# Optimization experiments

Hardware: AMD Instinct MI355X
Metric: run time of the kernel (lower is better)

The kernel has to match this reference:

```python
import jax, jax.numpy as jnp
import numpy as np

B, S = 8, 2048

def setup_inputs() -> dict:
    key = jax.random.key(0)
    ks = iter(jax.random.split(key, 64))
    def lin(din, dout):
        w = jax.random.normal(next(ks), (din, dout), jnp.float32) / np.float32(np.sqrt(din))
        b = jax.random.normal(next(ks), (dout,), jnp.float32) * 0.01
        return w, b
    inp = {}
    inp['x'] = jax.random.normal(next(ks), (B, S, 256), jnp.float32)
    def blk(tag, d, ff):
        for name, (din, dout) in [('q',(d,d)),('k',(d,d)),('v',(d,d)),('o',(d,d)),('ff1',(d,ff)),('ff2',(ff,d))]:
            w, b = lin(din, dout)
            inp[f'{name}_w{tag}'] = w; inp[f'{name}_b{tag}'] = b
        inp[f'ln1_g{tag}'] = jnp.ones((d,), jnp.float32); inp[f'ln1_b{tag}'] = jnp.zeros((d,), jnp.float32)
        inp[f'ln2_g{tag}'] = jnp.ones((d,), jnp.float32); inp[f'ln2_b{tag}'] = jnp.zeros((d,), jnp.float32)
    blk(1, 256, 1024)
    blk(2, 128, 512)
    for nm, (din, dout) in [('dr1',(256,128)),('dr2',(128,64)),('dr3',(64,32)),('dr4',(32,14))]:
        w, b = lin(din, dout)
        inp[f'{nm}_w'] = w; inp[f'{nm}_b'] = b
    return inp

def _ln(x, g, b, eps=1e-5):
    m = x.mean(-1, keepdims=True)
    v = ((x - m) ** 2).mean(-1, keepdims=True)
    return (x - m) / jnp.sqrt(v + eps) * g + b

def _mha(x, wq, bq, wk, bk, wv, bv, wo, bo, h):
    Bx, Sx, D = x.shape
    hd = D // h
    q = (x @ wq + bq).reshape(Bx, Sx, h, hd).transpose(0, 2, 1, 3)
    k = (x @ wk + bk).reshape(Bx, Sx, h, hd).transpose(0, 2, 1, 3)
    v = (x @ wv + bv).reshape(Bx, Sx, h, hd).transpose(0, 2, 1, 3)
    scores = jnp.einsum('bhqd,bhkd->bhqk', q, k) / jnp.sqrt(jnp.float32(hd))  # [B,h,S,S]
    p = jax.nn.softmax(scores, axis=-1)
    o = jnp.einsum('bhqk,bhkd->bqhd', p, v).reshape(Bx, Sx, D)
    return o @ wo + bo

def _encoder(x, p, h):
    a = _mha(x, p['qw'], p['qb'], p['kw'], p['kb'], p['vw'], p['vb'], p['ow'], p['ob'], h)
    x = _ln(a + x, p['g1'], p['b1'])
    f = jax.nn.relu(x @ p['fw1'] + p['fb1']) @ p['fw2'] + p['fb2']
    return _ln(f + x, p['g2'], p['b2'])

def _pe(s, d):
    pos = jnp.arange(s, dtype=jnp.float32)[:, None]
    dep = jnp.arange(d, dtype=jnp.float32)[None, :]
    ang = pos / jnp.power(jnp.float32(10000.0), dep / d)
    even = (jnp.arange(d)[None, :] % 2) == 0
    return jnp.where(even, jnp.sin(ang), jnp.cos(ang))

def _forward(x,
             q_w1, q_b1, k_w1, k_b1, v_w1, v_b1, o_w1, o_b1,
             ff1_w1, ff1_b1, ff2_w1, ff2_b1, ln1_g1, ln1_b1, ln2_g1, ln2_b1,
             dr1_w, dr1_b,
             q_w2, q_b2, k_w2, k_b2, v_w2, v_b2, o_w2, o_b2,
             ff1_w2, ff1_b2, ff2_w2, ff2_b2, ln1_g2, ln1_b2, ln2_g2, ln2_b2,
             dr2_w, dr2_b, dr3_w, dr3_b, dr4_w, dr4_b):
    h = x + _pe(x.shape[1], x.shape[2])
    p1 = dict(qw=q_w1, qb=q_b1, kw=k_w1, kb=k_b1, vw=v_w1, vb=v_b1, ow=o_w1, ob=o_b1,
              fw1=ff1_w1, fb1=ff1_b1, fw2=ff2_w1, fb2=ff2_b1, g1=ln1_g1, b1=ln1_b1, g2=ln2_g1, b2=ln2_b1)
    h = _encoder(h, p1, 8)
    h = h @ dr1_w + dr1_b
    p2 = dict(qw=q_w2, qb=q_b2, kw=k_w2, kb=k_b2, vw=v_w2, vb=v_b2, ow=o_w2, ob=o_b2,
              fw1=ff1_w2, fb1=ff1_b2, fw2=ff2_w2, fb2=ff2_b2, g1=ln1_g2, b1=ln1_b2, g2=ln2_g2, b2=ln2_b2)
    h = _encoder(h, p2, 8)
    h = h @ dr2_w + dr2_b
    h = jnp.max(h, axis=1)  # AdaptiveMaxPool1d(1) over the sequence dim -> [B, 64]
    h = h @ dr3_w + dr3_b
    return h @ dr4_w + dr4_b  # [B, 14]

def reference(x,
              q_w1, q_b1, k_w1, k_b1, v_w1, v_b1, o_w1, o_b1,
              ff1_w1, ff1_b1, ff2_w1, ff2_b1, ln1_g1, ln1_b1, ln2_g1, ln2_b1,
              dr1_w, dr1_b,
              q_w2, q_b2, k_w2, k_b2, v_w2, v_b2, o_w2, o_b2,
              ff1_w2, ff1_b2, ff2_w2, ff2_b2, ln1_g2, ln1_b2, ln2_g2, ln2_b2,
              dr2_w, dr2_b, dr3_w, dr3_b, dr4_w, dr4_b):
    return _forward(x,
                    q_w1, q_b1, k_w1, k_b1, v_w1, v_b1, o_w1, o_b1,
                    ff1_w1, ff1_b1, ff2_w1, ff2_b1, ln1_g1, ln1_b1, ln2_g1, ln2_b1,
                    dr1_w, dr1_b,
                    q_w2, q_b2, k_w2, k_b2, v_w2, v_b2, o_w2, o_b2,
                    ff1_w2, ff1_b2, ff2_w2, ff2_b2, ln1_g2, ln1_b2, ln2_g2, ln2_b2,
                    dr2_w, dr2_b, dr3_w, dr3_b, dr4_w, dr4_b)
```

## Files before the change

kernel.cpp:

```cpp
#include <hip/hip_runtime.h>
#include <hip/hip_bf16.h>
#include <math.h>

#define SEQ  2048
#define BATCH 8
#define NTOK (SEQ*BATCH)

typedef __attribute__((ext_vector_type(8))) short short8v;
typedef __attribute__((ext_vector_type(4))) float f32x4;
typedef unsigned short u16;

__device__ __forceinline__ u16 f2bf(float f) {
    __hip_bfloat16 h = __float2bfloat16(f);
    return *reinterpret_cast<u16*>(&h);
}

struct WDescs {
    const float* src[13];
    int K[13];
    int N[13];
    long dst[13];
    float scale[13];
    int tstart[14];
};

__global__ __launch_bounds__(256) void convert_w_kernel(WDescs d, u16* __restrict__ WA) {
    __shared__ float tile[64][65];
    int blk = blockIdx.x;
    int di = 0;
    while (di < 12 && blk >= d.tstart[di + 1]) ++di;
    int t  = blk - d.tstart[di];
    int K  = d.K[di], N = d.N[di];
    int tn = N >> 6;
    int k0 = (t / tn) << 6, n0 = (t % tn) << 6;
    const float* src = d.src[di];
    float sc = d.scale[di];
    int tid = threadIdx.x;
    #pragma unroll
    for (int i = 0; i < 16; ++i) {
        int id = i * 256 + tid;
        int kk = id >> 6, nn = id & 63;
        tile[kk][nn] = src[(size_t)(k0 + kk) * N + n0 + nn];
    }
    __syncthreads();
    u16* dst = WA + d.dst[di];
    #pragma unroll
    for (int i = 0; i < 16; ++i) {
        int id = i * 256 + tid;
        int nn = id >> 6, kk = id & 63;
        dst[(size_t)(n0 + nn) * K + k0 + kk] = f2bf(tile[kk][nn] * sc);
    }
}

__global__ __launch_bounds__(256) void convert_bias_kernel(
    const float* qb1, const float* kb1, const float* vb1,
    const float* qb2, const float* kb2, const float* vb2,
    float* __restrict__ BA, float qs1, float qs2)
{
    int t = blockIdx.x * 256 + threadIdx.x;
    if      (t < 256)  BA[t] = qb1[t] * qs1;
    else if (t < 512)  BA[t] = kb1[t - 256];
    else if (t < 768)  BA[t] = vb1[t - 512];
    else if (t < 896)  BA[t] = qb2[t - 768] * qs2;
    else if (t < 1024) BA[t] = kb2[t - 896];
    else if (t < 1152) BA[t] = vb2[t - 1024];
}

__global__ __launch_bounds__(256) void add_pe_kernel(const float* __restrict__ x,
                                                     float* __restrict__ h,
                                                     u16* __restrict__ hb) {
    int idx = blockIdx.x * 256 + threadIdx.x;
    int s = idx >> 8;
    int d = idx & 255;
    float p   = powf(10000.0f, (float)d * (1.0f / 256.0f));
    float ang = (float)s / p;
    float pe  = (d & 1) ? cosf(ang) : sinf(ang);
    #pragma unroll
    for (int b = 0; b < BATCH; ++b) {
        size_t g = ((size_t)(b * SEQ + s) << 8) + d;
        float v = x[g] + pe;
        h[g]  = v;
        hb[g] = f2bf(v);
    }
}

template<int RELU, int WF32, int WBF16>
__global__ __launch_bounds__(256) void gemm_bf16_kernel(
    const u16* __restrict__ A, const u16* __restrict__ Bt,
    const float* __restrict__ bias, float* __restrict__ Cf,
    u16* __restrict__ Cb, int N, int K)
{
    __shared__ u16 As[2][128 * 64];
    __shared__ u16 Bs[2][128 * 64];
    const int tid  = threadIdx.x;
    const int lane = tid & 63;
    const int c    = lane & 15, g = lane >> 4;
    const int w    = tid >> 6;
    const int wr   = w >> 1, wc = w & 1;
    const size_t bm = (size_t)blockIdx.y * 128;
    const size_t bn = (size_t)blockIdx.x * 128;

    f32x4 acc[4][4];
    #pragma unroll
    for (int i = 0; i < 4; ++i)
        #pragma unroll
        for (int j = 0; j < 4; ++j) acc[i][j] = (f32x4){0.f, 0.f, 0.f, 0.f};

    auto stage = [&](int buf, int t) {
        #pragma unroll
        for (int j = 0; j < 4; ++j) {
            int cid = j * 256 + tid;
            int row = cid >> 3, blk = cid & 7;
            int lofs = row * 64 + ((blk ^ (row & 7)) * 8);
            short8v av = *(const short8v*)&A[(bm + row) * K + t * 64 + blk * 8];
            *(short8v*)&As[buf][lofs] = av;
            short8v bv = *(const short8v*)&Bt[(bn + row) * K + t * 64 + blk * 8];
            *(short8v*)&Bs[buf][lofs] = bv;
        }
    };

    const int nt = K >> 6;
    stage(0, 0);
    __syncthreads();
    for (int t = 0; t < nt; ++t) {
        if (t + 1 < nt) stage((t + 1) & 1, t + 1);
        const int bfi = t & 1;
        #pragma unroll
        for (int ks2 = 0; ks2 < 2; ++ks2) {
            short8v af[4], bfr[4];
            #pragma unroll
            for (int am = 0; am < 4; ++am) {
                int r = wr * 64 + am * 16 + c;
                af[am] = *(const short8v*)&As[bfi][r * 64 + (((ks2 * 4 + g) ^ (r & 7)) * 8)];
            }
            #pragma unroll
            for (int bn_ = 0; bn_ < 4; ++bn_) {
                int r = wc * 64 + bn_ * 16 + c;
                bfr[bn_] = *(const short8v*)&Bs[bfi][r * 64 + (((ks2 * 4 + g) ^ (r & 7)) * 8)];
            }
            #pragma unroll
            for (int am = 0; am < 4; ++am)
                #pragma unroll
                for (int bn_ = 0; bn_ < 4; ++bn_)
                    acc[am][bn_] = __builtin_amdgcn_mfma_f32_16x16x32_bf16(
                                       af[am], bfr[bn_], acc[am][bn_], 0, 0, 0);
        }
        __syncthreads();
    }

    float bv[4];
    #pragma unroll
    for (int bn_ = 0; bn_ < 4; ++bn_) bv[bn_] = bias[bn + wc * 64 + bn_ * 16 + c];
    #pragma unroll
    for (int am = 0; am < 4; ++am) {
        #pragma unroll
        for (int bn_ = 0; bn_ < 4; ++bn_) {
            #pragma unroll
            for (int i = 0; i < 4; ++i) {
                size_t row = bm + wr * 64 + am * 16 + 4 * g + i;
                size_t col = bn + wc * 64 + bn_ * 16 + c;
                float v = acc[am][bn_][i] + bv[bn_];
                if (RELU) v = fmaxf(v, 0.f);
                if (WF32)  Cf[row * N + col] = v;
                if (WBF16) Cb[row * N + col] = f2bf(v);
            }
        }
    }
}

template<int RELU>
__global__ __launch_bounds__(256) void gemm_bias_kernel(
    const float* __restrict__ A, const float* __restrict__ W,
    const float* __restrict__ bias, float* __restrict__ C,
    int M, int N, int K)
{
    __shared__ float As[16][72];
    __shared__ float Bs[16][72];
    const int bm  = blockIdx.y * 64;
    const int bn  = blockIdx.x * 64;
    const int tid = threadIdx.x;
    const int tx  = tid & 15, ty = tid >> 4;

    float acc[4][4] = {{0.f}};

    for (int k0 = 0; k0 < K; k0 += 16) {
        #pragma unroll
        for (int i = 0; i < 4; ++i) {
            int f = tid + 256 * i;
            int row = f >> 4, kk = f & 15;
            As[kk][row] = A[(size_t)(bm + row) * K + k0 + kk];
        }
        #pragma unroll
        for (int i = 0; i < 4; ++i) {
            int f = tid + 256 * i;
            int kk = f >> 6, n = f & 63;
            Bs[kk][n] = W[(size_t)(k0 + kk) * N + bn + n];
        }
        __syncthreads();
        #pragma unroll
        for (int kk = 0; kk < 16; ++kk) {
            float4 a4 = *(const float4*)&As[kk][ty * 4];
            float4 b4 = *(const float4*)&Bs[kk][tx * 4];
            float av[4] = {a4.x, a4.y, a4.z, a4.w};
            float bw[4] = {b4.x, b4.y, b4.z, b4.w};
            #pragma unroll
            for (int i = 0; i < 4; ++i)
                #pragma unroll
                for (int j = 0; j < 4; ++j)
                    acc[i][j] = fmaf(av[i], bw[j], acc[i][j]);
        }
        __syncthreads();
    }

    float4 b4 = *(const float4*)&bias[bn + tx * 4];
    float bw[4] = {b4.x, b4.y, b4.z, b4.w};
    #pragma unroll
    for (int i = 0; i < 4; ++i) {
        int row = bm + ty * 4 + i;
        float4 o;
        float v0 = acc[i][0] + bw[0];
        float v1 = acc[i][1] + bw[1];
        float v2 = acc[i][2] + bw[2];
        float v3 = acc[i][3] + bw[3];
        if (RELU) {
            v0 = fmaxf(v0, 0.f); v1 = fmaxf(v1, 0.f);
            v2 = fmaxf(v2, 0.f); v3 = fmaxf(v3, 0.f);
        }
        o.x = v0; o.y = v1; o.z = v2; o.w = v3;
        *(float4*)&C[(size_t)row * N + bn + tx * 4] = o;
    }
}

template<int D, int WBF>
__global__ __launch_bounds__(256) void ln_residual_kernel(
    const float* __restrict__ a, const float* __restrict__ r,
    const float* __restrict__ g, const float* __restrict__ bb,
    float* __restrict__ out, u16* __restrict__ outb)
{
    const int N = D >> 6;
    int wave = threadIdx.x >> 6;
    int lane = threadIdx.x & 63;
    size_t token = (size_t)blockIdx.x * 4 + wave;
    const float* ar = a + token * D;
    const float* rr = r + token * D;

    float xv[N];
    float s = 0.f;
    #pragma unroll
    for (int i = 0; i < N; ++i) {
        int d = lane + (i << 6);
        xv[i] = ar[d] + rr[d];
        s += xv[i];
    }
    #pragma unroll
    for (int off = 1; off < 64; off <<= 1) s += __shfl_xor(s, off);
    float mean = s * (1.0f / D);
    float vs = 0.f;
    #pragma unroll
    for (int i = 0; i < N; ++i) { float d0 = xv[i] - mean; vs += d0 * d0; }
    #pragma unroll
    for (int off = 1; off < 64; off <<= 1) vs += __shfl_xor(vs, off);
    float inv = 1.0f / sqrtf(vs * (1.0f / D) + 1e-5f);
    #pragma unroll
    for (int i = 0; i < N; ++i) {
        int d = lane + (i << 6);
        float v = (xv[i] - mean) * inv * g[d] + bb[d];
        out[token * D + d] = v;
        if (WBF) outb[token * D + d] = f2bf(v);
    }
}

template<int HD>
__global__ __launch_bounds__(256) void flash_mfma_kernel(
    const u16* __restrict__ QKV, u16* __restrict__ Og)
{
    constexpr int D    = 8 * HD;
    constexpr int SD   = 3 * D;
    constexpr int NDH  = HD / 16;
    constexpr int KSTR = 40;
    constexpr int PSTR = 72;

    __shared__ u16 Ks[64 * KSTR];
    __shared__ u16 Vt[(NDH * 16) * PSTR];
    __shared__ u16 Pb[4 * 16 * PSTR];

    const int tid  = threadIdx.x;
    const int w    = tid >> 6;
    const int lane = tid & 63;
    const int c    = lane & 15;
    const int g    = lane >> 4;

    const int bh = blockIdx.y;
    const int b  = bh >> 3, hh = bh & 7;
    const size_t qvbase = (size_t)b * SEQ * SD + (size_t)hh * HD;
    const size_t obase  = (size_t)b * SEQ * D  + (size_t)hh * HD;
    const int qbase = blockIdx.x * 128;

    short8v qf[2];
    #pragma unroll
    for (int qb = 0; qb < 2; ++qb) {
        if (HD == 16 && g >= 2) {
            short8v z;
            #pragma unroll
            for (int i = 0; i < 8; ++i) z[i] = 0;
            qf[qb] = z;
        } else {
            int qrow = qbase + w * 32 + qb * 16 + c;
            qf[qb] = *(const short8v*)&QKV[qvbase + (size_t)qrow * SD + 8 * g];
        }
    }

    f32x4 oacc[2][NDH];
    float lreg[2][4];
    #pragma unroll
    for (int qb = 0; qb < 2; ++qb) {
        #pragma unroll
        for (int dh = 0; dh < NDH; ++dh) oacc[qb][dh] = (f32x4){0.f, 0.f, 0.f, 0.f};
        #pragma unroll
        for (int i = 0; i < 4; ++i) lreg[qb][i] = 0.f;
    }

    const int skey = tid >> 2;
    const int sch  = (tid & 3) * 8;
    const int spos = ((skey >> 5) << 5) + 2 * (skey & 15) + ((skey >> 4) & 1);

    for (int kt = 0; kt < SEQ; kt += 64) {
        __syncthreads();
        {
            short8v kv;
            if (HD == 16 && sch >= 16) {
                #pragma unroll
                for (int i = 0; i < 8; ++i) kv[i] = 0;
            } else {
                kv = *(const short8v*)&QKV[qvbase + (size_t)(kt + skey) * SD + D + sch];
            }
            *(short8v*)&Ks[skey * KSTR + sch] = kv;
        }
        if (!(HD == 16 && sch >= 16)) {
            short8v vv = *(const short8v*)&QKV[qvbase + (size_t)(kt + skey) * SD + 2 * D + sch];
            #pragma unroll
            for (int i = 0; i < 8; ++i)
                Vt[(sch + i) * PSTR + spos] = (u16)vv[i];
        }
        __syncthreads();

        short8v kf[4];
        #pragma unroll
        for (int kh = 0; kh < 4; ++kh)
            kf[kh] = *(const short8v*)&Ks[(16 * kh + c) * KSTR + 8 * g];
        short8v vf[NDH][2];
        #pragma unroll
        for (int dh = 0; dh < NDH; ++dh)
            #pragma unroll
            for (int kc = 0; kc < 2; ++kc)
                vf[dh][kc] = *(const short8v*)&Vt[(16 * dh + c) * PSTR + 32 * kc + 8 * g];

        #pragma unroll
        for (int qb = 0; qb < 2; ++qb) {
            f32x4 s[4];
            #pragma unroll
            for (int kh = 0; kh < 4; ++kh)
                s[kh] = __builtin_amdgcn_mfma_f32_16x16x32_bf16(
                            qf[qb], kf[kh], (f32x4){0.f, 0.f, 0.f, 0.f}, 0, 0, 0);

            unsigned* Pu = (unsigned*)Pb;
            #pragma unroll
            for (int i = 0; i < 4; ++i) {
                float p0 = exp2f(s[0][i]);
                float p1 = exp2f(s[1][i]);
                float p2 = exp2f(s[2][i]);
                float p3 = exp2f(s[3][i]);
                lreg[qb][i] += (p0 + p1) + (p2 + p3);
                int row = w * 16 + 4 * g + i;
                Pu[row * (PSTR / 2) + c]      = (unsigned)f2bf(p0) | ((unsigned)f2bf(p1) << 16);
                Pu[row * (PSTR / 2) + 16 + c] = (unsigned)f2bf(p2) | ((unsigned)f2bf(p3) << 16);
            }

            short8v pf0 = *(const short8v*)&Pb[(w * 16 + c) * PSTR + 8 * g];
            short8v pf1 = *(const short8v*)&Pb[(w * 16 + c) * PSTR + 32 + 8 * g];
            #pragma unroll
            for (int dh = 0; dh < NDH; ++dh) {
                oacc[qb][dh] = __builtin_amdgcn_mfma_f32_16x16x32_bf16(
                                   pf0, vf[dh][0], oacc[qb][dh], 0, 0, 0);
                oacc[qb][dh] = __builtin_amdgcn_mfma_f32_16x16x32_bf16(
                                   pf1, vf[dh][1], oacc[qb][dh], 0, 0, 0);
            }
        }
    }

    #pragma unroll
    for (int qb = 0; qb < 2; ++qb) {
        #pragma unroll
        for (int i = 0; i < 4; ++i) {
            float li = lreg[qb][i];
            li += __shfl_xor(li, 1);
            li += __shfl_xor(li, 2);
            li += __shfl_xor(li, 4);
            li += __shfl_xor(li, 8);
            float inv = 1.0f / li;
            int qrow = qbase + w * 32 + qb * 16 + 4 * g + i;
            #pragma unroll
            for (int dh = 0; dh < NDH; ++dh)
                Og[obase + (size_t)qrow * D + 16 * dh + c] = f2bf(oacc[qb][dh][i] * inv);
        }
    }
}

__global__ __launch_bounds__(256) void maxpool_kernel(const float* __restrict__ in,
                                                      float* __restrict__ out) {
    __shared__ float red[4][64];
    int b = blockIdx.x, d = threadIdx.x & 63, st = threadIdx.x >> 6;
    float m = -INFINITY;
    for (int s = st * (SEQ / 4); s < (st + 1) * (SEQ / 4); ++s)
        m = fmaxf(m, in[((size_t)b * SEQ + s) * 64 + d]);
    red[st][d] = m;
    __syncthreads();
    if (st == 0) {
        m = fmaxf(fmaxf(red[0][d], red[1][d]), fmaxf(red[2][d], red[3][d]));
        out[b * 64 + d] = m;
    }
}

__global__ __launch_bounds__(256) void head_kernel(
    const float* __restrict__ pooled,
    const float* __restrict__ w3, const float* __restrict__ b3,
    const float* __restrict__ w4, const float* __restrict__ b4,
    float* __restrict__ out)
{
    __shared__ float t[8][32];
    int tid = threadIdx.x;
    {
        int b = tid >> 5, j = tid & 31;
        float s = b3[j];
        #pragma unroll
        for (int k = 0; k < 64; ++k) s = fmaf(pooled[b * 64 + k], w3[k * 32 + j], s);
        t[b][j] = s;
    }
    __syncthreads();
    if (tid < 8 * 14) {
        int b = tid / 14, j = tid % 14;
        float s = b4[j];
        #pragma unroll
        for (int k = 0; k < 32; ++k) s = fmaf(t[b][k], w4[k * 14 + j], s);
        out[b * 14 + j] = s;
    }
}

extern "C" void kernel_launch(void* const* d_in, const int* in_sizes, int n_in,
                              void* d_out, int out_size, void* d_ws, size_t ws_size,
                              hipStream_t stream) {
    const float* x     = (const float*)d_in[0];
    const float* qw1   = (const float*)d_in[1];
    const float* qb1   = (const float*)d_in[2];
    const float* kw1   = (const float*)d_in[3];
    const float* kb1   = (const float*)d_in[4];
    const float* vw1   = (const float*)d_in[5];
    const float* vb1   = (const float*)d_in[6];
    const float* ow1   = (const float*)d_in[7];
    const float* ob1   = (const float*)d_in[8];
    const float* f1w1  = (const float*)d_in[9];
    const float* f1b1  = (const float*)d_in[10];
    const float* f2w1  = (const float*)d_in[11];
    const float* f2b1  = (const float*)d_in[12];
    const float* ln1g1 = (const float*)d_in[13];
    const float* ln1b1 = (const float*)d_in[14];
    const float* ln2g1 = (const float*)d_in[15];
    const float* ln2b1 = (const float*)d_in[16];
    const float* qw2   = (const float*)d_in[17];
    const float* qb2   = (const float*)d_in[18];
    const float* kw2   = (const float*)d_in[19];
    const float* kb2   = (const float*)d_in[20];
    const float* vw2   = (const float*)d_in[21];
    const float* vb2   = (const float*)d_in[22];
    const float* ow2   = (const float*)d_in[23];
    const float* ob2   = (const float*)d_in[24];
    const float* f1w2  = (const float*)d_in[25];
    const float* f1b2  = (const float*)d_in[26];
    const float* f2w2  = (const float*)d_in[27];
    const float* f2b2  = (const float*)d_in[28];
    const float* ln1g2 = (const float*)d_in[29];
    const float* ln1b2 = (const float*)d_in[30];
    const float* ln2g2 = (const float*)d_in[31];
    const float* ln2b2 = (const float*)d_in[32];
    const float* dr1w  = (const float*)d_in[33];
    const float* dr1b  = (const float*)d_in[34];
    const float* dr2w  = (const float*)d_in[35];
    const float* dr2b  = (const float*)d_in[36];
    const float* dr3w  = (const float*)d_in[37];
    const float* dr3b  = (const float*)d_in[38];
    const float* dr4w  = (const float*)d_in[39];
    const float* dr4b  = (const float*)d_in[40];

    const size_t T = NTOK;
    float* F1 = (float*)d_ws;
    float* F2 = F1 + T * 256;
    u16*   E1 = (u16*)(F2 + T * 256);
    u16*   E2 = E1 + T * 256;
    u16*   E3 = E2 + T * 256;
    u16*   Dq = E3 + T * 256;
    u16*   WA = Dq + T * 1024;
    float* BA = (float*)(WA + 1048576);

    const float QS1 = 0.25503488f;
    const float QS2 = 0.36067376f;

    WDescs wd;
    const float* srcs[13] = {qw1, kw1, vw1, ow1, f1w1, f2w1, dr1w,
                             qw2, kw2, vw2, ow2, f1w2, f2w2};
    int Ks_[13]  = {256, 256, 256, 256, 256, 1024, 256, 128, 128, 128, 128, 128, 512};
    int Ns_[13]  = {256, 256, 256, 256, 1024, 256, 128, 128, 128, 128, 128, 512, 128};
    long dsts[13] = {0, 65536, 131072, 196608, 262144, 524288, 786432,
                     819200, 835584, 851968, 868352, 884736, 950272};
    float scs[13] = {QS1, 1.f, 1.f, 1.f, 1.f, 1.f, 1.f, QS2, 1.f, 1.f, 1.f, 1.f, 1.f};
    int tst[14] = {0, 16, 32, 48, 64, 128, 192, 200, 204, 208, 212, 216, 232, 248};
    for (int i = 0; i < 13; ++i) {
        wd.src[i] = srcs[i]; wd.K[i] = Ks_[i]; wd.N[i] = Ns_[i];
        wd.dst[i] = dsts[i]; wd.scale[i] = scs[i];
    }
    for (int i = 0; i < 14; ++i) wd.tstart[i] = tst[i];

    const dim3 blk(256);

    convert_w_kernel<<<248, blk, 0, stream>>>(wd, WA);
    convert_bias_kernel<<<5, blk, 0, stream>>>(qb1, kb1, vb1, qb2, kb2, vb2, BA, QS1, QS2);

    add_pe_kernel<<<SEQ, blk, 0, stream>>>(x, F1, E1);

    gemm_bf16_kernel<0,0,1><<<dim3(6, 128), blk, 0, stream>>>(E1, WA + 0,      BA,   nullptr, Dq, 768, 256);
    flash_mfma_kernel<32><<<dim3(16, 64), blk, 0, stream>>>(Dq, E2);
    gemm_bf16_kernel<0,1,0><<<dim3(2, 128), blk, 0, stream>>>(E2, WA + 196608, ob1,  F2, nullptr, 256, 256);
    ln_residual_kernel<256,1><<<NTOK / 4, blk, 0, stream>>>(F2, F1, ln1g1, ln1b1, F1, E1);
    gemm_bf16_kernel<1,0,1><<<dim3(8, 128), blk, 0, stream>>>(E1, WA + 262144, f1b1, nullptr, Dq, 1024, 256);
    gemm_bf16_kernel<0,1,0><<<dim3(2, 128), blk, 0, stream>>>(Dq, WA + 524288, f2b1, F2, nullptr, 256, 1024);
    ln_residual_kernel<256,1><<<NTOK / 4, blk, 0, stream>>>(F2, F1, ln2g1, ln2b1, F1, E1);

    gemm_bf16_kernel<0,1,1><<<dim3(1, 128), blk, 0, stream>>>(E1, WA + 786432, dr1b, F2, E2, 128, 256);

    gemm_bf16_kernel<0,0,1><<<dim3(3, 128), blk, 0, stream>>>(E2, WA + 819200, BA + 768, nullptr, Dq, 384, 128);
    flash_mfma_kernel<16><<<dim3(16, 64), blk, 0, stream>>>(Dq, E3);
    gemm_bf16_kernel<0,1,0><<<dim3(1, 128), blk, 0, stream>>>(E3, WA + 868352, ob2,  F1, nullptr, 128, 128);
    ln_residual_kernel<128,1><<<NTOK / 4, blk, 0, stream>>>(F1, F2, ln1g2, ln1b2, F2, E1);
    gemm_bf16_kernel<1,0,1><<<dim3(4, 128), blk, 0, stream>>>(E1, WA + 884736, f1b2, nullptr, Dq, 512, 128);
    gemm_bf16_kernel<0,1,0><<<dim3(1, 128), blk, 0, stream>>>(Dq, WA + 950272, f2b2, F1, nullptr, 128, 512);
    ln_residual_kernel<128,0><<<NTOK / 4, blk, 0, stream>>>(F1, F2, ln2g2, ln2b2, F2, E1);

    gemm_bias_kernel<0><<<dim3(1, NTOK / 64), blk, 0, stream>>>(F2, dr2w, dr2b, F1, NTOK, 64, 128);
    maxpool_kernel<<<BATCH, blk, 0, stream>>>(F1, F2);
    head_kernel<<<1, blk, 0, stream>>>(F2, dr3w, dr3b, dr4w, dr4b, (float*)d_out);
}
```

Measured before the change: 599.5 us.

## Use direct-to-LDS loads, double-buffer flash K/V, move dr2 projection to MFMA GEMM

```diff
diff --git a/kernel.cpp b/kernel.cpp
--- a/kernel.cpp
+++ b/kernel.cpp
@@ -14,21 +14,30 @@
     __hip_bfloat16 h = __float2bfloat16(f);
     return *reinterpret_cast<u16*>(&h);
 }
+__device__ __forceinline__ unsigned pack_bf2(float a, float b) {
+    __hip_bfloat162 h = __float22bfloat162_rn(float2{a, b});
+    return *reinterpret_cast<unsigned*>(&h);
+}
+__device__ __forceinline__ void gl_lds16(const u16* g, u16* l) {
+    __builtin_amdgcn_global_load_lds(
+        (const __attribute__((address_space(1))) unsigned int*)g,
+        (__attribute__((address_space(3))) unsigned int*)l, 16, 0, 0);
+}
 
 struct WDescs {
-    const float* src[13];
-    int K[13];
-    int N[13];
-    long dst[13];
-    float scale[13];
-    int tstart[14];
+    const float* src[14];
+    int K[14];
+    int N[14];
+    long dst[14];
+    float scale[14];
+    int tstart[15];
 };
 
 __global__ __launch_bounds__(256) void convert_w_kernel(WDescs d, u16* __restrict__ WA) {
     __shared__ float tile[64][65];
     int blk = blockIdx.x;
     int di = 0;
-    while (di < 12 && blk >= d.tstart[di + 1]) ++di;
+    while (di < 13 && blk >= d.tstart[di + 1]) ++di;
     int t  = blk - d.tstart[di];
     int K  = d.K[di], N = d.N[di];
     int tn = N >> 6;
@@ -55,7 +64,7 @@
 __global__ __launch_bounds__(256) void convert_bias_kernel(
     const float* qb1, const float* kb1, const float* vb1,
     const float* qb2, const float* kb2, const float* vb2,
-    float* __restrict__ BA, float qs1, float qs2)
+    const float* dr2b, float* __restrict__ BA, float qs1, float qs2)
 {
     int t = blockIdx.x * 256 + threadIdx.x;
     if      (t < 256)  BA[t] = qb1[t] * qs1;
@@ -64,6 +73,8 @@
     else if (t < 896)  BA[t] = qb2[t - 768] * qs2;
     else if (t < 1024) BA[t] = kb2[t - 896];
     else if (t < 1152) BA[t] = vb2[t - 1024];
+    else if (t < 1216) BA[t] = dr2b[t - 1152];
+    else if (t < 1280) BA[t] = 0.f;
 }
 
 __global__ __launch_bounds__(256) void add_pe_kernel(const float* __restrict__ x,
@@ -72,9 +83,9 @@
     int idx = blockIdx.x * 256 + threadIdx.x;
     int s = idx >> 8;
     int d = idx & 255;
-    float p   = powf(10000.0f, (float)d * (1.0f / 256.0f));
-    float ang = (float)s / p;
-    float pe  = (d & 1) ? cosf(ang) : sinf(ang);
+    float inv = exp2f((float)d * -0.0519051264732f);
+    float ang = (float)s * inv;
+    float pe  = (d & 1) ? __cosf(ang) : __sinf(ang);
     #pragma unroll
     for (int b = 0; b < BATCH; ++b) {
         size_t g = ((size_t)(b * SEQ + s) << 8) + d;
@@ -90,8 +101,8 @@
     const float* __restrict__ bias, float* __restrict__ Cf,
     u16* __restrict__ Cb, int N, int K)
 {
-    __shared__ u16 As[2][128 * 64];
-    __shared__ u16 Bs[2][128 * 64];
+    __shared__ u16 As[128 * 64];
+    __shared__ u16 Bs[128 * 64];
     const int tid  = threadIdx.x;
     const int lane = tid & 63;
     const int c    = lane & 15, g = lane >> 4;
@@ -106,37 +117,29 @@
         #pragma unroll
         for (int j = 0; j < 4; ++j) acc[i][j] = (f32x4){0.f, 0.f, 0.f, 0.f};
 
-    auto stage = [&](int buf, int t) {
+    const int nt = K >> 6;
+    for (int t = 0; t < nt; ++t) {
         #pragma unroll
         for (int j = 0; j < 4; ++j) {
             int cid = j * 256 + tid;
             int row = cid >> 3, blk = cid & 7;
-            int lofs = row * 64 + ((blk ^ (row & 7)) * 8);
-            short8v av = *(const short8v*)&A[(bm + row) * K + t * 64 + blk * 8];
-            *(short8v*)&As[buf][lofs] = av;
-            short8v bv = *(const short8v*)&Bt[(bn + row) * K + t * 64 + blk * 8];
-            *(short8v*)&Bs[buf][lofs] = bv;
-        }
-    };
-
-    const int nt = K >> 6;
-    stage(0, 0);
-    __syncthreads();
-    for (int t = 0; t < nt; ++t) {
-        if (t + 1 < nt) stage((t + 1) & 1, t + 1);
-        const int bfi = t & 1;
+            int sof = (blk ^ (row & 7)) * 8;
+            gl_lds16(&A [(bm + row) * K + t * 64 + sof], &As[cid * 8]);
+            gl_lds16(&Bt[(bn + row) * K + t * 64 + sof], &Bs[cid * 8]);
+        }
+        __syncthreads();
         #pragma unroll
         for (int ks2 = 0; ks2 < 2; ++ks2) {
             short8v af[4], bfr[4];
             #pragma unroll
             for (int am = 0; am < 4; ++am) {
                 int r = wr * 64 + am * 16 + c;
-                af[am] = *(const short8v*)&As[bfi][r * 64 + (((ks2 * 4 + g) ^ (r & 7)) * 8)];
+                af[am] = *(const short8v*)&As[r * 64 + (((ks2 * 4 + g) ^ (r & 7)) * 8)];
             }
             #pragma unroll
             for (int bn_ = 0; bn_ < 4; ++bn_) {
                 int r = wc * 64 + bn_ * 16 + c;
-                bfr[bn_] = *(const short8v*)&Bs[bfi][r * 64 + (((ks2 * 4 + g) ^ (r & 7)) * 8)];
+                bfr[bn_] = *(const short8v*)&Bs[r * 64 + (((ks2 * 4 + g) ^ (r & 7)) * 8)];
             }
             #pragma unroll
             for (int am = 0; am < 4; ++am)
@@ -165,69 +168,6 @@
                 if (WBF16) Cb[row * N + col] = f2bf(v);
             }
         }
-    }
-}
-
-template<int RELU>
-__global__ __launch_bounds__(256) void gemm_bias_kernel(
-    const float* __restrict__ A, const float* __restrict__ W,
-    const float* __restrict__ bias, float* __restrict__ C,
-    int M, int N, int K)
-{
-    __shared__ float As[16][72];
-    __shared__ float Bs[16][72];
-    const int bm  = blockIdx.y * 64;
-    const int bn  = blockIdx.x * 64;
-    const int tid = threadIdx.x;
-    const int tx  = tid & 15, ty = tid >> 4;
-
-    float acc[4][4] = {{0.f}};
-
-    for (int k0 = 0; k0 < K; k0 += 16) {
-        #pragma unroll
-        for (int i = 0; i < 4; ++i) {
-            int f = tid + 256 * i;
-            int row = f >> 4, kk = f & 15;
-            As[kk][row] = A[(size_t)(bm + row) * K + k0 + kk];
-        }
-        #pragma unroll
-        for (int i = 0; i < 4; ++i) {
-            int f = tid + 256 * i;
-            int kk = f >> 6, n = f & 63;
-            Bs[kk][n] = W[(size_t)(k0 + kk) * N + bn + n];
-        }
-        __syncthreads();
-        #pragma unroll
-        for (int kk = 0; kk < 16; ++kk) {
-            float4 a4 = *(const float4*)&As[kk][ty * 4];
-            float4 b4 = *(const float4*)&Bs[kk][tx * 4];
-            float av[4] = {a4.x, a4.y, a4.z, a4.w};
-            float bw[4] = {b4.x, b4.y, b4.z, b4.w};
-            #pragma unroll
-            for (int i = 0; i < 4; ++i)
-                #pragma unroll
-                for (int j = 0; j < 4; ++j)
-                    acc[i][j] = fmaf(av[i], bw[j], acc[i][j]);
-        }
-        __syncthreads();
-    }
-
-    float4 b4 = *(const float4*)&bias[bn + tx * 4];
-    float bw[4] = {b4.x, b4.y, b4.z, b4.w};
-    #pragma unroll
-    for (int i = 0; i < 4; ++i) {
-        int row = bm + ty * 4 + i;
-        float4 o;
-        float v0 = acc[i][0] + bw[0];
-        float v1 = acc[i][1] + bw[1];
-        float v2 = acc[i][2] + bw[2];
-        float v3 = acc[i][3] + bw[3];
-        if (RELU) {
-            v0 = fmaxf(v0, 0.f); v1 = fmaxf(v1, 0.f);
-            v2 = fmaxf(v2, 0.f); v3 = fmaxf(v3, 0.f);
-        }
-        o.x = v0; o.y = v1; o.z = v2; o.w = v3;
-        *(float4*)&C[(size_t)row * N + bn + tx * 4] = o;
     }
 }
 
@@ -274,15 +214,13 @@
 __global__ __launch_bounds__(256) void flash_mfma_kernel(
     const u16* __restrict__ QKV, u16* __restrict__ Og)
 {
-    constexpr int D    = 8 * HD;
-    constexpr int SD   = 3 * D;
-    constexpr int NDH  = HD / 16;
-    constexpr int KSTR = 40;
-    constexpr int PSTR = 72;
-
-    __shared__ u16 Ks[64 * KSTR];
-    __shared__ u16 Vt[(NDH * 16) * PSTR];
-    __shared__ u16 Pb[4 * 16 * PSTR];
+    constexpr int D   = 8 * HD;
+    constexpr int SD  = 3 * D;
+    constexpr int NDH = HD / 16;
+
+    __shared__ u16 Ks[2][64 * 32];
+    __shared__ u16 Vt[2][NDH * 16 * 64];
+    __shared__ u16 Pb[64 * 64];
 
     const int tid  = threadIdx.x;
     const int w    = tid >> 6;
@@ -290,19 +228,19 @@
     const int c    = lane & 15;
     const int g    = lane >> 4;
 
-    const int bh = blockIdx.y;
-    const int b  = bh >> 3, hh = bh & 7;
+    const int H    = blockIdx.x + (blockIdx.y << 4);
+    const int bh   = H & 63;
+    const int qblk = H >> 6;
+    const int b = bh >> 3, hh = bh & 7;
     const size_t qvbase = (size_t)b * SEQ * SD + (size_t)hh * HD;
     const size_t obase  = (size_t)b * SEQ * D  + (size_t)hh * HD;
-    const int qbase = blockIdx.x * 128;
+    const int qbase = qblk * 128;
 
     short8v qf[2];
     #pragma unroll
     for (int qb = 0; qb < 2; ++qb) {
         if (HD == 16 && g >= 2) {
-            short8v z;
-            #pragma unroll
-            for (int i = 0; i < 8; ++i) z[i] = 0;
+            short8v z = {0, 0, 0, 0, 0, 0, 0, 0};
             qf[qb] = z;
         } else {
             int qrow = qbase + w * 32 + qb * 16 + c;
@@ -323,37 +261,43 @@
     const int skey = tid >> 2;
     const int sch  = (tid & 3) * 8;
     const int spos = ((skey >> 5) << 5) + 2 * (skey & 15) + ((skey >> 4) & 1);
-
-    for (int kt = 0; kt < SEQ; kt += 64) {
-        __syncthreads();
-        {
-            short8v kv;
-            if (HD == 16 && sch >= 16) {
-                #pragma unroll
-                for (int i = 0; i < 8; ++i) kv[i] = 0;
-            } else {
-                kv = *(const short8v*)&QKV[qvbase + (size_t)(kt + skey) * SD + D + sch];
-            }
-            *(short8v*)&Ks[skey * KSTR + sch] = kv;
-        }
-        if (!(HD == 16 && sch >= 16)) {
-            short8v vv = *(const short8v*)&QKV[qvbase + (size_t)(kt + skey) * SD + 2 * D + sch];
-            #pragma unroll
-            for (int i = 0; i < 8; ++i)
-                Vt[(sch + i) * PSTR + spos] = (u16)vv[i];
-        }
-        __syncthreads();
+    const int squad = spos >> 3, soff = spos & 7;
+    const bool vstager = !(HD == 16 && sch >= 16);
+    const int vkc = (c & 7) ^ ((c & 8) >> 1);
+
+    gl_lds16(&QKV[qvbase + (size_t)skey * SD + D + sch], &Ks[0][tid * 8]);
+    if (vstager) {
+        short8v v0 = *(const short8v*)&QKV[qvbase + (size_t)skey * SD + 2 * D + sch];
+        #pragma unroll
+        for (int i = 0; i < 8; ++i) {
+            int row = sch + i;
+            int vk = (row & 7) ^ ((row & 8) >> 1);
+            Vt[0][row * 64 + ((squad ^ vk) << 3) + soff] = (u16)v0[i];
+        }
+    }
+    __syncthreads();
+
+    int buf = 0;
+    const int NT = SEQ / 64;
+    for (int t = 0; t < NT; ++t) {
+        short8v vv = {0, 0, 0, 0, 0, 0, 0, 0};
+        const bool pre = (t + 1 < NT);
+        if (pre) {
+            const size_t nb = qvbase + (size_t)((t + 1) * 64 + skey) * SD;
+            if (vstager) vv = *(const short8v*)&QKV[nb + 2 * D + sch];
+            gl_lds16(&QKV[nb + D + sch], &Ks[buf ^ 1][tid * 8]);
+        }
 
         short8v kf[4];
         #pragma unroll
         for (int kh = 0; kh < 4; ++kh)
-            kf[kh] = *(const short8v*)&Ks[(16 * kh + c) * KSTR + 8 * g];
-        short8v vf[NDH][2];
-        #pragma unroll
-        for (int dh = 0; dh < NDH; ++dh)
-            #pragma unroll
-            for (int kc = 0; kc < 2; ++kc)
-                vf[dh][kc] = *(const short8v*)&Vt[(16 * dh + c) * PSTR + 32 * kc + 8 * g];
+            kf[kh] = *(const short8v*)&Ks[buf][(16 * kh + c) * 32 + 8 * g];
+        short8v vfr[NDH][2];
+        #pragma unroll
+        for (int dh = 0; dh < NDH; ++dh) {
+            vfr[dh][0] = *(const short8v*)&Vt[buf][(16 * dh + c) * 64 + ((g ^ vkc) << 3)];
+            vfr[dh][1] = *(const short8v*)&Vt[buf][(16 * dh + c) * 64 + (((4 + g) ^ vkc) << 3)];
+        }
 
         #pragma unroll
         for (int qb = 0; qb < 2; ++qb) {
@@ -363,7 +307,6 @@
                 s[kh] = __builtin_amdgcn_mfma_f32_16x16x32_bf16(
                             qf[qb], kf[kh], (f32x4){0.f, 0.f, 0.f, 0.f}, 0, 0, 0);
 
-            unsigned* Pu = (unsigned*)Pb;
             #pragma unroll
             for (int i = 0; i < 4; ++i) {
                 float p0 = exp2f(s[0][i]);
@@ -371,21 +314,34 @@
                 float p2 = exp2f(s[2][i]);
                 float p3 = exp2f(s[3][i]);
                 lreg[qb][i] += (p0 + p1) + (p2 + p3);
-                int row = w * 16 + 4 * g + i;
-                Pu[row * (PSTR / 2) + c]      = (unsigned)f2bf(p0) | ((unsigned)f2bf(p1) << 16);
-                Pu[row * (PSTR / 2) + 16 + c] = (unsigned)f2bf(p2) | ((unsigned)f2bf(p3) << 16);
+                int rr = 4 * g + i;
+                int pk = (rr & 7) ^ ((rr & 8) >> 1);
+                int base = (w * 16 + rr) * 64 + 2 * (c & 3);
+                *(unsigned*)&Pb[base + (((c >> 2) ^ pk) << 3)]       = pack_bf2(p0, p1);
+                *(unsigned*)&Pb[base + ((((c >> 2) + 4) ^ pk) << 3)] = pack_bf2(p2, p3);
             }
 
-            short8v pf0 = *(const short8v*)&Pb[(w * 16 + c) * PSTR + 8 * g];
-            short8v pf1 = *(const short8v*)&Pb[(w * 16 + c) * PSTR + 32 + 8 * g];
+            short8v pf0 = *(const short8v*)&Pb[(w * 16 + c) * 64 + ((g ^ vkc) << 3)];
+            short8v pf1 = *(const short8v*)&Pb[(w * 16 + c) * 64 + (((4 + g) ^ vkc) << 3)];
             #pragma unroll
             for (int dh = 0; dh < NDH; ++dh) {
                 oacc[qb][dh] = __builtin_amdgcn_mfma_f32_16x16x32_bf16(
-                                   pf0, vf[dh][0], oacc[qb][dh], 0, 0, 0);
+                                   pf0, vfr[dh][0], oacc[qb][dh], 0, 0, 0);
                 oacc[qb][dh] = __builtin_amdgcn_mfma_f32_16x16x32_bf16(
-                                   pf1, vf[dh][1], oacc[qb][dh], 0, 0, 0);
+                                   pf1, vfr[dh][1], oacc[qb][dh], 0, 0, 0);
             }
         }
+
+        if (pre && vstager) {
+            #pragma unroll
+            for (int i = 0; i < 8; ++i) {
+                int row = sch + i;
+                int vk = (row & 7) ^ ((row & 8) >> 1);
+                Vt[buf ^ 1][row * 64 + ((squad ^ vk) << 3) + soff] = (u16)vv[i];
+            }
+        }
+        __syncthreads();
+        buf ^= 1;
     }
 
     #pragma unroll
@@ -412,7 +368,7 @@
     int b = blockIdx.x, d = threadIdx.x & 63, st = threadIdx.x >> 6;
     float m = -INFINITY;
     for (int s = st * (SEQ / 4); s < (st + 1) * (SEQ / 4); ++s)
-        m = fmaxf(m, in[((size_t)b * SEQ + s) * 64 + d]);
+        m = fmaxf(m, in[((size_t)b * SEQ + s) * 128 + d]);
     red[st][d] = m;
     __syncthreads();
     if (st == 0) {
@@ -505,24 +461,24 @@
     const float QS2 = 0.36067376f;
 
     WDescs wd;
-    const float* srcs[13] = {qw1, kw1, vw1, ow1, f1w1, f2w1, dr1w,
-                             qw2, kw2, vw2, ow2, f1w2, f2w2};
-    int Ks_[13]  = {256, 256, 256, 256, 256, 1024, 256, 128, 128, 128, 128, 128, 512};
-    int Ns_[13]  = {256, 256, 256, 256, 1024, 256, 128, 128, 128, 128, 128, 512, 128};
-    long dsts[13] = {0, 65536, 131072, 196608, 262144, 524288, 786432,
-                     819200, 835584, 851968, 868352, 884736, 950272};
-    float scs[13] = {QS1, 1.f, 1.f, 1.f, 1.f, 1.f, 1.f, QS2, 1.f, 1.f, 1.f, 1.f, 1.f};
-    int tst[14] = {0, 16, 32, 48, 64, 128, 192, 200, 204, 208, 212, 216, 232, 248};
-    for (int i = 0; i < 13; ++i) {
+    const float* srcs[14] = {qw1, kw1, vw1, ow1, f1w1, f2w1, dr1w,
+                             qw2, kw2, vw2, ow2, f1w2, f2w2, dr2w};
+    int Ks_[14]  = {256, 256, 256, 256, 256, 1024, 256, 128, 128, 128, 128, 128, 512, 128};
+    int Ns_[14]  = {256, 256, 256, 256, 1024, 256, 128, 128, 128, 128, 128, 512, 128, 64};
+    long dsts[14] = {0, 65536, 131072, 196608, 262144, 524288, 786432,
+                     819200, 835584, 851968, 868352, 884736, 950272, 1015808};
+    float scs[14] = {QS1, 1.f, 1.f, 1.f, 1.f, 1.f, 1.f, QS2, 1.f, 1.f, 1.f, 1.f, 1.f, 1.f};
+    int tst[15] = {0, 16, 32, 48, 64, 128, 192, 200, 204, 208, 212, 216, 232, 248, 250};
+    for (int i = 0; i < 14; ++i) {
         wd.src[i] = srcs[i]; wd.K[i] = Ks_[i]; wd.N[i] = Ns_[i];
         wd.dst[i] = dsts[i]; wd.scale[i] = scs[i];
     }
-    for (int i = 0; i < 14; ++i) wd.tstart[i] = tst[i];
+    for (int i = 0; i < 15; ++i) wd.tstart[i] = tst[i];
 
     const dim3 blk(256);
 
-    convert_w_kernel<<<248, blk, 0, stream>>>(wd, WA);
-    convert_bias_kernel<<<5, blk, 0, stream>>>(qb1, kb1, vb1, qb2, kb2, vb2, BA, QS1, QS2);
+    convert_w_kernel<<<250, blk, 0, stream>>>(wd, WA);
+    convert_bias_kernel<<<5, blk, 0, stream>>>(qb1, kb1, vb1, qb2, kb2, vb2, dr2b, BA, QS1, QS2);
 
     add_pe_kernel<<<SEQ, blk, 0, stream>>>(x, F1, E1);
 
@@ -542,9 +498,9 @@
     ln_residual_kernel<128,1><<<NTOK / 4, blk, 0, stream>>>(F1, F2, ln1g2, ln1b2, F2, E1);
     gemm_bf16_kernel<1,0,1><<<dim3(4, 128), blk, 0, stream>>>(E1, WA + 884736, f1b2, nullptr, Dq, 512, 128);
     gemm_bf16_kernel<0,1,0><<<dim3(1, 128), blk, 0, stream>>>(Dq, WA + 950272, f2b2, F1, nullptr, 128, 512);
-    ln_residual_kernel<128,0><<<NTOK / 4, blk, 0, stream>>>(F1, F2, ln2g2, ln2b2, F2, E1);
-
-    gemm_bias_kernel<0><<<dim3(1, NTOK / 64), blk, 0, stream>>>(F2, dr2w, dr2b, F1, NTOK, 64, 128);
+    ln_residual_kernel<128,1><<<NTOK / 4, blk, 0, stream>>>(F1, F2, ln2g2, ln2b2, F2, E1);
+
+    gemm_bf16_kernel<0,1,0><<<dim3(1, 128), blk, 0, stream>>>(E1, WA + 1015808, BA + 1152, F1, nullptr, 128, 128);
     maxpool_kernel<<<BATCH, blk, 0, stream>>>(F1, F2);
     head_kernel<<<1, blk, 0, stream>>>(F2, dr3w, dr3b, dr4w, dr4b, (float*)d_out);
 }
```

New measurement: 603.6 us. Within noise of the previous version (+0.7%).
